# Performance work log

Hardware: AMD Instinct MI355X
Metric: run time of the kernel (lower is better)

The kernel has to match this reference:

```python
import jax, jax.numpy as jnp
import numpy as np

B, E, H, N, L, K = 32, 1024, 1024, 128, 64, 8


def setup_inputs() -> dict:
    key = jax.random.key(0)
    ks = jax.random.split(key, 9)
    s = 0.02
    inputs = jax.random.normal(ks[0], (B, E), dtype=jnp.float32)
    Wq = jax.random.normal(ks[1], (H, E), dtype=jnp.float32) * s
    bq = jnp.zeros((H,), dtype=jnp.float32)
    Wk = jax.random.normal(ks[2], (H, H), dtype=jnp.float32) * s
    bk = jnp.zeros((H,), dtype=jnp.float32)
    Wc = jax.random.normal(ks[3], (H, 2 * H), dtype=jnp.float32) * s
    bc = jnp.zeros((H,), dtype=jnp.float32)
    # per-batch-item cache: N slots, each slot has a [dk] key and a [L, H] value ('zone')
    cache_keys = jax.random.normal(ks[4], (B, N, E), dtype=jnp.float32)
    cache_values = jax.random.normal(ks[5], (B, N, L, H), dtype=jnp.float32)
    return {
        "inputs": inputs,
        "Wq": Wq, "bq": bq,
        "Wk": Wk, "bk": bk,
        "Wc": Wc, "bc": bc,
        "cache_keys": cache_keys,
        "cache_values": cache_values,
    }


def reference(inputs, Wq, bq, Wk, bk, Wc, bc, cache_keys, cache_values):
    # Cache retrieval: score each slot against the input, take top-K,
    # softmax the top-K scores into mixture weights.
    scores = jnp.einsum('bne,be->bn', cache_keys, inputs)          # [B, N]
    top_scores, top_idx = jax.lax.top_k(scores, K)                 # [B, K]
    weights = jax.nn.softmax(top_scores, axis=-1)                  # [B, K]
    zones = jnp.take_along_axis(
        cache_values, top_idx[:, :, None, None], axis=1)           # [B, K, L, H]

    # attention_wq(inputs[i]) -> query; attention_wk(zone) -> keys
    query = inputs @ Wq.T + bq                                     # [B, H]
    keys = jnp.einsum('bklh,gh->bklg', zones, Wk) + bk             # [B, K, L, H]

    # scaled dot-product attention of query over each zone's L positions
    inv_sqrt = jnp.float32(1.0 / np.sqrt(H))
    attn_logits = jnp.einsum('bh,bklh->bkl', query, keys) * inv_sqrt
    attn = jax.nn.softmax(attn_logits, axis=-1)                    # [B, K, L]
    per_zone_out = jnp.einsum('bkl,bklh->bkh', attn, zones)        # [B, K, H]

    # weighted sum over retrieved zones
    attention_output = jnp.einsum('bk,bkh->bh', weights, per_zone_out)  # [B, H]

    # fuse with input and project
    fused = jnp.concatenate([attention_output, inputs], axis=-1)   # [B, 2H]
    hidden_states = fused @ Wc.T + bc                              # [B, H]
    return hidden_states
```

## Files before the change

### kernel.cpp

```cpp
#include <hip/hip_runtime.h>
#include <math.h>

#define NB 32
#define NE 1024
#define NH 1024
#define NN 128
#define NL 64
#define NK 8
#define GS 8

__device__ __forceinline__ float dot4f(float4 a, float4 b) {
    return a.x * b.x + a.y * b.y + a.z * b.z + a.w * b.w;
}

__device__ __forceinline__ float4 add4(float4 a, float4 b) {
    return make_float4(a.x + b.x, a.y + b.y, a.z + b.z, a.w + b.w);
}

template <int D>
__device__ void rowdot8(const float* __restrict__ A, const float* __restrict__ W,
                        const float* __restrict__ bias, float* __restrict__ C,
                        int wid) {
    int lane = threadIdx.x & 63;
    int o  = wid >> 2;
    int b0 = (wid & 3) * 8;
    const float4* Wr = (const float4*)(W + (size_t)o * D);
    const float4* Ar[8];
#pragma unroll
    for (int i = 0; i < 8; ++i) Ar[i] = (const float4*)(A + (size_t)(b0 + i) * D);
    float acc[8] = {0.f, 0.f, 0.f, 0.f, 0.f, 0.f, 0.f, 0.f};
#pragma unroll
    for (int c = 0; c < D / 256; ++c) {
        float4 w4 = Wr[c * 64 + lane];
#pragma unroll
        for (int i = 0; i < 8; ++i) acc[i] += dot4f(w4, Ar[i][c * 64 + lane]);
    }
#pragma unroll
    for (int s = 32; s; s >>= 1)
#pragma unroll
        for (int i = 0; i < 8; ++i) acc[i] += __shfl_down(acc[i], s, 64);
    if (lane == 0) {
        float bb = bias[o];
#pragma unroll
        for (int i = 0; i < 8; ++i) C[(size_t)(b0 + i) * NH + o] = acc[i] + bb;
    }
}

__global__ __launch_bounds__(256)
void fat1_kernel(const float* __restrict__ cache_keys,
                 const float* __restrict__ inputs,
                 const float* __restrict__ Wq,
                 const float* __restrict__ bq,
                 float* __restrict__ scores,
                 float* __restrict__ query) {
    if (blockIdx.x < 1024) {
        int wid  = blockIdx.x * 4 + (threadIdx.x >> 6);
        int lane = threadIdx.x & 63;
        int b = wid >> 7, n = wid & 127;
        const float4* ck = (const float4*)(cache_keys + ((size_t)b * NN + n) * NE);
        const float4* in = (const float4*)(inputs + (size_t)b * NE);
        float acc = 0.f;
#pragma unroll
        for (int c = 0; c < 4; ++c) acc += dot4f(ck[c * 64 + lane], in[c * 64 + lane]);
#pragma unroll
        for (int s = 32; s; s >>= 1) acc += __shfl_down(acc, s, 64);
        if (lane == 0) scores[b * NN + n] = acc;
    } else {
        int wid = (blockIdx.x - 1024) * 4 + (threadIdx.x >> 6);
        rowdot8<1024>(inputs, Wq, bq, query, wid);
    }
}

__global__ __launch_bounds__(256)
void fat2_kernel(const float* __restrict__ query,
                 const float* __restrict__ Wk,
                 const float* __restrict__ scores,
                 float* __restrict__ pqk,
                 int* __restrict__ top_idx,
                 float* __restrict__ weights) {
    __shared__ float qlds[128 * 8];
    __shared__ float red[8 * 32 * 8];
    __shared__ float tv[NK];
    int t = threadIdx.x;
    if (blockIdx.x < 1024) {
        int gs = blockIdx.x & 7;
        int hs = (blockIdx.x >> 3) & 31;
        int bg = blockIdx.x >> 8;
        int b0 = bg * 8;
#pragma unroll
        for (int j = 0; j < 4; ++j) {
            int idx = t * 4 + j;
            int g = idx >> 3, bj = idx & 7;
            qlds[idx] = query[(size_t)(b0 + bj) * NH + gs * 128 + g];
        }
        __syncthreads();
        int h_local = t & 31, g_lane = t >> 5;
        int h = hs * 32 + h_local;
        float acc[8] = {0.f, 0.f, 0.f, 0.f, 0.f, 0.f, 0.f, 0.f};
#pragma unroll
        for (int i = 0; i < 16; ++i) {
            int g_local = g_lane * 16 + i;
            float w = Wk[(size_t)(gs * 128 + g_local) * NH + h];
            float4 q0 = *(const float4*)&qlds[g_local * 8];
            float4 q1 = *(const float4*)&qlds[g_local * 8 + 4];
            acc[0] += q0.x * w; acc[1] += q0.y * w; acc[2] += q0.z * w; acc[3] += q0.w * w;
            acc[4] += q1.x * w; acc[5] += q1.y * w; acc[6] += q1.z * w; acc[7] += q1.w * w;
        }
        *(float4*)&red[(g_lane * 32 + h_local) * 8]     = *(float4*)&acc[0];
        *(float4*)&red[(g_lane * 32 + h_local) * 8 + 4] = *(float4*)&acc[4];
        __syncthreads();
        int bj = t >> 5, hl = t & 31;
        float ssum = 0.f;
#pragma unroll
        for (int gl = 0; gl < 8; ++gl) ssum += red[(gl * 32 + hl) * 8 + bj];
        pqk[((size_t)gs * NB + b0 + bj) * NH + hs * 32 + hl] = ssum;
    } else {
        int b = blockIdx.x - 1024;
        if (t < 64) {
            float s0 = scores[b * NN + t];
            float s1 = scores[b * NN + 64 + t];
            for (int i = 0; i < NK; ++i) {
                float v = s0; int idx = t;
                if (s1 > v) { v = s1; idx = t + 64; }
#pragma unroll
                for (int s = 1; s < 64; s <<= 1) {
                    float ov = __shfl_xor(v, s, 64);
                    int   oi = __shfl_xor(idx, s, 64);
                    if (ov > v || (ov == v && oi < idx)) { v = ov; idx = oi; }
                }
                if (t == 0) { tv[i] = v; top_idx[b * NK + i] = idx; }
                if (idx == t)      s0 = -INFINITY;
                if (idx == t + 64) s1 = -INFINITY;
            }
        }
        __syncthreads();
        if (t < NK) {
            float e = __expf(tv[t] - tv[0]);
            float sum = e;
            sum += __shfl_xor(sum, 1, 64);
            sum += __shfl_xor(sum, 2, 64);
            sum += __shfl_xor(sum, 4, 64);
            weights[b * NK + t] = e / sum;
        }
    }
}

__global__ __launch_bounds__(256)
void attn_kernel(const float* __restrict__ pqk,
                 const float* __restrict__ cache_values,
                 const int* __restrict__ top_idx,
                 const float* __restrict__ weights,
                 float* __restrict__ patt) {
    int b = blockIdx.x >> 3, k = blockIdx.x & 7;
    __shared__ float qk_lds[NH];
    __shared__ float logits[NL];
    __shared__ float coef[NL];
    int t = threadIdx.x;

    {
        float4 s = make_float4(0.f, 0.f, 0.f, 0.f);
#pragma unroll
        for (int gs = 0; gs < GS; ++gs) {
            float4 p = ((const float4*)pqk)[((size_t)gs * NB + b) * 256 + t];
            s.x += p.x; s.y += p.y; s.z += p.z; s.w += p.w;
        }
        ((float4*)qk_lds)[t] = s;
    }
    __syncthreads();

    int lane = t & 63, wv = t >> 6;
    int zi = top_idx[b * NK + k];
    const float* zbase = cache_values + (((size_t)b * NN + zi) * NL) * NH;

    {
        float4 qk[4];
#pragma unroll
        for (int c = 0; c < 4; ++c) qk[c] = ((const float4*)qk_lds)[c * 64 + lane];
#pragma unroll
        for (int rp = 0; rp < 8; ++rp) {
            int l0 = wv * 16 + rp;
            int l1 = l0 + 8;
            const float4* zr0 = (const float4*)(zbase + (size_t)l0 * NH);
            const float4* zr1 = (const float4*)(zbase + (size_t)l1 * NH);
            float4 z0[4], z1[4];
#pragma unroll
            for (int c = 0; c < 4; ++c) { z0[c] = zr0[c * 64 + lane]; z1[c] = zr1[c * 64 + lane]; }
            float d0 = 0.f, d1 = 0.f;
#pragma unroll
            for (int c = 0; c < 4; ++c) { d0 += dot4f(z0[c], qk[c]); d1 += dot4f(z1[c], qk[c]); }
#pragma unroll
            for (int s = 32; s; s >>= 1) {
                d0 += __shfl_down(d0, s, 64);
                d1 += __shfl_down(d1, s, 64);
            }
            if (lane == 0) {
                logits[l0] = d0 * 0.03125f;
                logits[l1] = d1 * 0.03125f;
            }
        }
    }
    __syncthreads();

    if (t < 64) {
        float v = logits[t];
        float m = v;
#pragma unroll
        for (int s = 1; s < 64; s <<= 1) m = fmaxf(m, __shfl_xor(m, s, 64));
        float e = __expf(v - m);
        float sum = e;
#pragma unroll
        for (int s = 1; s < 64; s <<= 1) sum += __shfl_xor(sum, s, 64);
        coef[t] = weights[b * NK + k] * e / sum;
    }
    __syncthreads();

    {
        float4 acc = make_float4(0.f, 0.f, 0.f, 0.f);
#pragma unroll
        for (int lb = 0; lb < 8; ++lb) {
            float4 z[8];
#pragma unroll
            for (int j = 0; j < 8; ++j)
                z[j] = ((const float4*)(zbase + (size_t)(lb * 8 + j) * NH))[t];
#pragma unroll
            for (int j = 0; j < 8; ++j) {
                float c = coef[lb * 8 + j];
                acc.x += c * z[j].x; acc.y += c * z[j].y;
                acc.z += c * z[j].z; acc.w += c * z[j].w;
            }
        }
        ((float4*)patt)[((size_t)b * NK + k) * 256 + t] = acc;
    }
}

__global__ __launch_bounds__(256)
void finalbf_kernel(const float* __restrict__ patt,
                    const float* __restrict__ inputs,
                    const float* __restrict__ Wc,
                    const float* __restrict__ bc,
                    float* __restrict__ out) {
    __shared__ float4 sF[4][256];
    __shared__ float4 sIn[4][256];
    int t = threadIdx.x;
    int bg = blockIdx.x >> 5, og = blockIdx.x & 31;
    int b0 = bg * 4, o0 = og * 32;

#pragma unroll
    for (int i = 0; i < 4; ++i) {
        const float4* pb = (const float4*)(patt + (size_t)(b0 + i) * NK * NH);
        float4 v = pb[t];
#pragma unroll
        for (int k = 1; k < NK; ++k) v = add4(v, pb[k * 256 + t]);
        sF[i][t] = v;
        sIn[i][t] = ((const float4*)(inputs + (size_t)(b0 + i) * NE))[t];
    }
    __syncthreads();

    int lane = t & 63, wv = t >> 6;
    float acc[4][8];
#pragma unroll
    for (int i = 0; i < 4; ++i)
#pragma unroll
        for (int j = 0; j < 8; ++j) acc[i][j] = 0.f;

    const float4* WcBase = (const float4*)Wc;
#pragma unroll
    for (int c = 0; c < 8; ++c) {
        float4 a[4];
#pragma unroll
        for (int i = 0; i < 4; ++i)
            a[i] = (c < 4) ? sF[i][c * 64 + lane] : sIn[i][(c - 4) * 64 + lane];
#pragma unroll
        for (int j = 0; j < 8; ++j) {
            int o = o0 + wv * 8 + j;
            float4 w4 = WcBase[(size_t)o * 512 + c * 64 + lane];
#pragma unroll
            for (int i = 0; i < 4; ++i) acc[i][j] += dot4f(w4, a[i]);
        }
    }
#pragma unroll
    for (int s = 32; s; s >>= 1)
#pragma unroll
        for (int i = 0; i < 4; ++i)
#pragma unroll
            for (int j = 0; j < 8; ++j) acc[i][j] += __shfl_down(acc[i][j], s, 64);
    if (lane == 0) {
#pragma unroll
        for (int j = 0; j < 8; ++j) {
            int o = o0 + wv * 8 + j;
            float bb = bc[o];
#pragma unroll
            for (int i = 0; i < 4; ++i)
                out[(size_t)(b0 + i) * NH + o] = acc[i][j] + bb;
        }
    }
}

extern "C" void kernel_launch(void* const* d_in, const int* in_sizes, int n_in,
                              void* d_out, int out_size, void* d_ws, size_t ws_size,
                              hipStream_t stream) {
    const float* inputs       = (const float*)d_in[0];
    const float* Wq           = (const float*)d_in[1];
    const float* bq           = (const float*)d_in[2];
    const float* Wk           = (const float*)d_in[3];
    const float* Wc           = (const float*)d_in[5];
    const float* bc           = (const float*)d_in[6];
    const float* cache_keys   = (const float*)d_in[7];
    const float* cache_values = (const float*)d_in[8];
    float* out = (float*)d_out;

    float* ws      = (float*)d_ws;
    float* scores  = ws;
    float* query   = scores + 4096;
    float* pqk     = query + 32768;
    float* patt    = pqk + 262144;
    float* weights = patt + 262144;
    int*   tidx    = (int*)(weights + 256);
    (void)ws_size; (void)n_in; (void)in_sizes; (void)out_size;

    fat1_kernel<<<2048, 256, 0, stream>>>(cache_keys, inputs, Wq, bq, scores, query);
    fat2_kernel<<<1056, 256, 0, stream>>>(query, Wk, scores, pqk, tidx, weights);
    attn_kernel<<<NB * NK, 256, 0, stream>>>(pqk, cache_values, tidx, weights, patt);
    finalbf_kernel<<<256, 256, 0, stream>>>(patt, inputs, Wc, bc, out);
}
```

Baseline: 55.14 us.

## Fuse zone logits, softmax and weighted sum into a single pass

```diff
diff --git a/kernel.cpp b/kernel.cpp
--- a/kernel.cpp
+++ b/kernel.cpp
@@ -153,8 +153,8 @@
                  float* __restrict__ patt) {
     int b = blockIdx.x >> 3, k = blockIdx.x & 7;
     __shared__ float qk_lds[NH];
-    __shared__ float logits[NL];
-    __shared__ float coef[NL];
+    __shared__ float4 psum[4][256];
+    __shared__ float dsum_s[4];
     int t = threadIdx.x;
 
     {
@@ -172,64 +172,55 @@
     int zi = top_idx[b * NK + k];
     const float* zbase = cache_values + (((size_t)b * NN + zi) * NL) * NH;
 
+    float4 qk[4];
+#pragma unroll
+    for (int c = 0; c < 4; ++c) qk[c] = ((const float4*)qk_lds)[c * 64 + lane];
+
+    float4 acc[4];
+#pragma unroll
+    for (int c = 0; c < 4; ++c) acc[c] = make_float4(0.f, 0.f, 0.f, 0.f);
+    float dsum = 0.f;
+
+#pragma unroll
+    for (int rp = 0; rp < 8; ++rp) {
+        int l0 = wv * 16 + rp;
+        int l1 = l0 + 8;
+        const float4* zr0 = (const float4*)(zbase + (size_t)l0 * NH);
+        const float4* zr1 = (const float4*)(zbase + (size_t)l1 * NH);
+        float4 z0[4], z1[4];
+#pragma unroll
+        for (int c = 0; c < 4; ++c) { z0[c] = zr0[c * 64 + lane]; z1[c] = zr1[c * 64 + lane]; }
+        float d0 = 0.f, d1 = 0.f;
+#pragma unroll
+        for (int c = 0; c < 4; ++c) { d0 += dot4f(z0[c], qk[c]); d1 += dot4f(z1[c], qk[c]); }
+#pragma unroll
+        for (int s = 1; s < 64; s <<= 1) {
+            d0 += __shfl_xor(d0, s, 64);
+            d1 += __shfl_xor(d1, s, 64);
+        }
+        float p0 = __expf(d0 * 0.03125f);
+        float p1 = __expf(d1 * 0.03125f);
+        dsum += p0 + p1;
+#pragma unroll
+        for (int c = 0; c < 4; ++c) {
+            acc[c].x += p0 * z0[c].x + p1 * z1[c].x;
+            acc[c].y += p0 * z0[c].y + p1 * z1[c].y;
+            acc[c].z += p0 * z0[c].z + p1 * z1[c].z;
+            acc[c].w += p0 * z0[c].w + p1 * z1[c].w;
+        }
+    }
+
+#pragma unroll
+    for (int c = 0; c < 4; ++c) psum[wv][c * 64 + lane] = acc[c];
+    if (lane == 0) dsum_s[wv] = dsum;
+    __syncthreads();
+
     {
-        float4 qk[4];
-#pragma unroll
-        for (int c = 0; c < 4; ++c) qk[c] = ((const float4*)qk_lds)[c * 64 + lane];
-#pragma unroll
-        for (int rp = 0; rp < 8; ++rp) {
-            int l0 = wv * 16 + rp;
-            int l1 = l0 + 8;
-            const float4* zr0 = (const float4*)(zbase + (size_t)l0 * NH);
-            const float4* zr1 = (const float4*)(zbase + (size_t)l1 * NH);
-            float4 z0[4], z1[4];
-#pragma unroll
-            for (int c = 0; c < 4; ++c) { z0[c] = zr0[c * 64 + lane]; z1[c] = zr1[c * 64 + lane]; }
-            float d0 = 0.f, d1 = 0.f;
-#pragma unroll
-            for (int c = 0; c < 4; ++c) { d0 += dot4f(z0[c], qk[c]); d1 += dot4f(z1[c], qk[c]); }
-#pragma unroll
-            for (int s = 32; s; s >>= 1) {
-                d0 += __shfl_down(d0, s, 64);
-                d1 += __shfl_down(d1, s, 64);
-            }
-            if (lane == 0) {
-                logits[l0] = d0 * 0.03125f;
-                logits[l1] = d1 * 0.03125f;
-            }
-        }
-    }
-    __syncthreads();
-
-    if (t < 64) {
-        float v = logits[t];
-        float m = v;
-#pragma unroll
-        for (int s = 1; s < 64; s <<= 1) m = fmaxf(m, __shfl_xor(m, s, 64));
-        float e = __expf(v - m);
-        float sum = e;
-#pragma unroll
-        for (int s = 1; s < 64; s <<= 1) sum += __shfl_xor(sum, s, 64);
-        coef[t] = weights[b * NK + k] * e / sum;
-    }
-    __syncthreads();
-
-    {
-        float4 acc = make_float4(0.f, 0.f, 0.f, 0.f);
-#pragma unroll
-        for (int lb = 0; lb < 8; ++lb) {
-            float4 z[8];
-#pragma unroll
-            for (int j = 0; j < 8; ++j)
-                z[j] = ((const float4*)(zbase + (size_t)(lb * 8 + j) * NH))[t];
-#pragma unroll
-            for (int j = 0; j < 8; ++j) {
-                float c = coef[lb * 8 + j];
-                acc.x += c * z[j].x; acc.y += c * z[j].y;
-                acc.z += c * z[j].z; acc.w += c * z[j].w;
-            }
-        }
-        ((float4*)patt)[((size_t)b * NK + k) * 256 + t] = acc;
+        float dtot = dsum_s[0] + dsum_s[1] + dsum_s[2] + dsum_s[3];
+        float scale = weights[b * NK + k] / dtot;
+        float4 v = add4(add4(psum[0][t], psum[1][t]), add4(psum[2][t], psum[3][t]));
+        v.x *= scale; v.y *= scale; v.z *= scale; v.w *= scale;
+        ((float4*)patt)[((size_t)b * NK + k) * 256 + t] = v;
     }
 }
 
```

Result: faster. 49.14 us (-10.9%).
